# Kernel tuning notes

Measured on AMD Instinct MI355X. Metric: run time of the kernel, lower is better.

## Reference

```python
import jax, jax.numpy as jnp
import numpy as np
from jax import lax

ROUTINGS = 3
SCALING = 2
NUM_CAPSULE = 8
NUM_ATOMS = 16
EPS = 1e-9


def squash(v):
    # SegCaps squash: v * |v|^2 / ((1+|v|^2) * |v|), norm over last axis
    sq = jnp.sum(v * v, axis=-1, keepdims=True)
    return v * sq / ((1.0 + sq) * jnp.sqrt(sq + EPS))


def setup_inputs() -> dict:
    key = jax.random.key(0)
    k1, k2 = jax.random.split(key)
    B, H, Wd, Cin, Ain = 4, 56, 56, 8, 32
    x = jax.random.normal(k1, (B, H, Wd, Cin, Ain), dtype=jnp.float32)
    # TF conv2d_transpose filter layout: [k, k, out_ch, in_ch]
    W = jax.random.normal(k2, (4, 4, NUM_CAPSULE * NUM_ATOMS, Ain), dtype=jnp.float32) * 0.05
    b = 0.1 * jnp.ones((1, 1, NUM_CAPSULE, NUM_ATOMS), dtype=jnp.float32)
    return {"x": x, "W": W, "b": b}


def reference(x, W, b):
    B, H, Wd, Cin, Ain = x.shape
    Cout, Aout = NUM_CAPSULE, NUM_ATOMS
    # [B,H,W,Cin,A] -> [Cin,B,H,W,A] -> [Cin*B,H,W,A]  (faithful to original ordering)
    xt = jnp.transpose(x, (3, 0, 1, 2, 4)).reshape(Cin * B, H, Wd, Ain)
    # TF conv2d_transpose, SAME padding, stride=scaling: out spatial = in * scaling
    out = lax.conv_transpose(
        xt, W, strides=(SCALING, SCALING), padding="SAME",
        dimension_numbers=("NHWC", "HWIO", "NHWC"), transpose_kernel=True)
    Hp, Wp = out.shape[1], out.shape[2]
    # votes: [B, Cin, Hp, Wp, Cout, Aout]  (faithful to original reshape)
    votes = out.reshape(B, Cin, Hp, Wp, Cout, Aout)
    biases = jnp.broadcast_to(b, (Hp, Wp, Cout, Aout))
    logits = jnp.zeros((B, Cin, Hp, Wp, Cout), dtype=x.dtype)
    act = None
    for i in range(ROUTINGS):
        route = jax.nn.softmax(logits, axis=-1)                      # [B,Cin,Hp,Wp,Cout]
        pre = jnp.einsum("bihwc,bihwca->bhwca", route, votes) + biases
        act = squash(pre)                                            # [B,Hp,Wp,Cout,Aout]
        if i < ROUTINGS - 1:
            logits = logits + jnp.einsum("bihwca,bhwca->bihwc", votes, act)
    return act
```

## Files before the change

### kernel.cpp

```cpp
#include <hip/hip_runtime.h>
#include <math.h>

#define CEPS 1e-9f

typedef _Float16 half8 __attribute__((ext_vector_type(8)));
typedef _Float16 h2 __attribute__((ext_vector_type(2)));
typedef __fp16 fp16x2 __attribute__((ext_vector_type(2)));
typedef float floatx16 __attribute__((ext_vector_type(16)));


template<int CTRL>
__device__ __forceinline__ float dpp_add(float v) {
    return v + __int_as_float(__builtin_amdgcn_update_dpp(
        0, __float_as_int(v), CTRL, 0xF, 0xF, false));
}
template<int CTRL>
__device__ __forceinline__ h2 dpp_add_h2(h2 v) {
    int t = __builtin_amdgcn_update_dpp(
        0, __builtin_bit_cast(int, v), CTRL, 0xF, 0xF, false);
    return v + __builtin_bit_cast(h2, t);
}
__device__ __forceinline__ h2 sum_i8_h2(h2 v) {
    v = dpp_add_h2<0xB1>(v);
    v = dpp_add_h2<0x4E>(v);
    v = dpp_add_h2<0x141>(v);
    return v;
}
__device__ __forceinline__ h2 pkrtz(float a, float b) {
    return __builtin_bit_cast(h2, __builtin_amdgcn_cvt_pkrtz(a, b));
}
__device__ __forceinline__ float fdot2(h2 a, h2 b, float c) {
    return __builtin_amdgcn_fdot2(__builtin_bit_cast(fp16x2, a),
                                  __builtin_bit_cast(fp16x2, b), c, false);
}
__device__ __forceinline__ h2 hsel(bool c, h2 a, h2 b) {
    int r = c ? __builtin_bit_cast(int, a) : __builtin_bit_cast(int, b);
    return __builtin_bit_cast(h2, r);
}

__global__ __launch_bounds__(256) void prep_w(const float* __restrict__ Wt,
                                              _Float16* __restrict__ wb) {
    int idx = blockIdx.x * 256 + threadIdx.x;
    int parity = idx >> 11;
    int s = (idx >> 8) & 7;
    int t = (idx >> 6) & 3;
    int l = idx & 63;
    int rh = parity >> 1, rw = parity & 1;
    int n = t * 32 + (l & 31);
    int h = l >> 5;
    int ci0 = ((s & 1) << 4) + (h << 3);
    int kh = ((s >> 2) << 1) + 1 - rh;
    int kw = (((s >> 1) & 1) << 1) + 1 - rw;
    const float* src = Wt + (((kh * 4 + kw) * 128 + n) << 5) + ci0;
    float4 w0 = *(const float4*)src;
    float4 w1 = *(const float4*)(src + 4);
    half8 hv;
    hv[0] = (_Float16)w0.x; hv[1] = (_Float16)w0.y;
    hv[2] = (_Float16)w0.z; hv[3] = (_Float16)w0.w;
    hv[4] = (_Float16)w1.x; hv[5] = (_Float16)w1.y;
    hv[6] = (_Float16)w1.z; hv[7] = (_Float16)w1.w;
    *(half8*)(wb + ((long)idx << 3)) = hv;
}

__global__ __launch_bounds__(256, 5) void caps_mfma(
    const float* __restrict__ x,
    const _Float16* __restrict__ wb,
    const float* __restrict__ bias,
    float* __restrict__ out)
{
    __shared__ __align__(16) unsigned char smem[16000];
    _Float16* xt = (_Float16*)smem;
    _Float16* scxh = (_Float16*)smem;

    const int tid = threadIdx.x;
    const int tile = blockIdx.x;
    const int tu = tile / 14, tv = tile - tu * 14;
    const int u0 = tu * 4, v0 = tv * 4;
    const int rh = blockIdx.y >> 1;
    const int rw = blockIdx.y & 1;
    const int bp = blockIdx.z;
    const _Float16* wsrc = wb + ((long)blockIdx.y << 14);

    #pragma unroll
    for (int it = 0; it < 4; ++it) {
        int idx = tid + (it << 8);
        if (idx < 800) {
            int cell = idx >> 5;
            int r = idx & 31;
            int i = r >> 2;
            int ci0 = (r & 3) << 3;
            int ri = cell / 5, rj = cell - ri * 5;
            int gi = u0 + rh - 1 + ri;
            int gj = v0 + rw - 1 + rj;
            float tmp[8] = {0.f, 0.f, 0.f, 0.f, 0.f, 0.f, 0.f, 0.f};
            if ((unsigned)gi < 56u && (unsigned)gj < 56u) {
                const float* src = x + (((i & 3) * 56 + gi) * 56 + gj) * 256
                                     + ((bp * 2 + (i >> 2)) << 5) + ci0;
                float4 a0 = *(const float4*)src;
                float4 a1 = *(const float4*)(src + 4);
                tmp[0] = a0.x; tmp[1] = a0.y; tmp[2] = a0.z; tmp[3] = a0.w;
                tmp[4] = a1.x; tmp[5] = a1.y; tmp[6] = a1.z; tmp[7] = a1.w;
            }
            half8 hv;
            #pragma unroll
            for (int j = 0; j < 8; ++j) hv[j] = (_Float16)tmp[j];
            *(half8*)(xt + (cell * 8 + i) * 40 + ci0) = hv;
        }
    }
    __syncthreads();

    const int l = tid & 63;
    const int w = tid >> 6;
    const int col = l & 31, h = l >> 5;
    const int invA = (l & 31) * 40 + (h << 3);

    h2 pf[4][8];
    #pragma unroll
    for (int half = 0; half < 2; ++half) {
        floatx16 acc0, acc1;
        #pragma unroll
        for (int j = 0; j < 16; ++j) { acc0[j] = 0.f; acc1[j] = 0.f; }
        const int tb = half << 1;
        #pragma unroll
        for (int s = 0; s < 8; ++s) {
            const int tkh = s >> 2;
            const int tkw = (s >> 1) & 1;
            const int row = w + 1 - tkh;
            int aoff = (row * 5 + 1 - tkw) * 320 + ((s & 1) << 4) + invA;
            asm("" : "+v"(aoff));
            half8 af = *(const half8*)(xt + aoff);
            half8 bf0 = *(const half8*)(wsrc + (((s * 4 + tb) * 64 + l) << 3));
            half8 bf1 = *(const half8*)(wsrc + (((s * 4 + tb + 1) * 64 + l) << 3));
            acc0 = __builtin_amdgcn_mfma_f32_32x32x16_f16(af, bf0, acc0, 0, 0, 0);
            acc1 = __builtin_amdgcn_mfma_f32_32x32x16_f16(af, bf1, acc1, 0, 0, 0);
        }
        #pragma unroll
        for (int m = 0; m < 8; ++m) {
            pf[tb][m]     = pkrtz(acc0[2 * m], acc0[2 * m + 1]);
            pf[tb + 1][m] = pkrtz(acc1[2 * m], acc1[2 * m + 1]);
        }
        __builtin_amdgcn_sched_barrier(0);
    }

    __syncthreads();

    _Float16* scb = scxh + w * (8 * 136);
    const int cI = l >> 3;
    const int iI = l & 7;

    h2 bq2[8];
    {
        const float* bpt = bias + (cI << 4);
        float4 b0 = *(const float4*)bpt;
        float4 b1 = *(const float4*)(bpt + 4);
        float4 b2 = *(const float4*)(bpt + 8);
        float4 b3 = *(const float4*)(bpt + 12);
        bq2[0] = pkrtz(b0.x, b0.y); bq2[1] = pkrtz(b0.z, b0.w);
        bq2[2] = pkrtz(b1.x, b1.y); bq2[3] = pkrtz(b1.z, b1.w);
        bq2[4] = pkrtz(b2.x, b2.y); bq2[5] = pkrtz(b2.z, b2.w);
        bq2[6] = pkrtz(b3.x, b3.y); bq2[7] = pkrtz(b3.z, b3.w);
    }
    const h2 c0125 = pkrtz(0.125f, 0.125f);

    #pragma unroll
    for (int pixl = 0; pixl < 4; ++pixl) {
        #pragma unroll
        for (int t = 0; t < 4; ++t)
            #pragma unroll
            for (int il = 0; il < 4; ++il) {
                h2 pp = pf[t][(pixl << 1) + (il >> 1)];
                _Float16 v = (il & 1) ? pp.y : pp.x;
                scb[((h << 2) + il) * 136 + t * 32 + col] = v;
            }

        const _Float16* rbh = scb + iI * 136 + (cI << 4);
        h2 va2[8];
        *(half8*)&va2[0] = *(const half8*)(rbh);
        *(half8*)&va2[4] = *(const half8*)(rbh + 8);

        h2 pre2[8];
        float lg;

        #pragma unroll
        for (int j = 0; j < 8; ++j) {
            h2 s2 = sum_i8_h2(va2[j]);
            pre2[j] = s2 * c0125 + bq2[j];
        }
        {
            float n0 = fdot2(pre2[0], pre2[0], 0.f);
            float n1 = fdot2(pre2[1], pre2[1], 0.f);
            float n2 = fdot2(pre2[2], pre2[2], 0.f);
            float n3 = fdot2(pre2[3], pre2[3], 0.f);
            n0 = fdot2(pre2[4], pre2[4], n0);
            n1 = fdot2(pre2[5], pre2[5], n1);
            n2 = fdot2(pre2[6], pre2[6], n2);
            n3 = fdot2(pre2[7], pre2[7], n3);
            float nq = (n0 + n1) + (n2 + n3);
            float sc = nq * __builtin_amdgcn_rcpf(1.f + nq)
                          * __builtin_amdgcn_rsqf(nq + CEPS);
            h2 sc2 = pkrtz(sc, sc);
            #pragma unroll
            for (int j = 0; j < 8; ++j) pre2[j] *= sc2;
            float d0 = fdot2(va2[0], pre2[0], 0.f);
            float d1 = fdot2(va2[1], pre2[1], 0.f);
            float d2 = fdot2(va2[2], pre2[2], 0.f);
            float d3 = fdot2(va2[3], pre2[3], 0.f);
            d0 = fdot2(va2[4], pre2[4], d0);
            d1 = fdot2(va2[5], pre2[5], d1);
            d2 = fdot2(va2[6], pre2[6], d2);
            d3 = fdot2(va2[7], pre2[7], d3);
            lg = (d0 + d1) + (d2 + d3);
        }

        #pragma unroll
        for (int r = 1; r < 3; ++r) {
            float e = __expf(lg);
            float ss = dpp_add<0x128>(e);
            ss += __int_as_float(__builtin_amdgcn_ds_swizzle(
                      __float_as_int(ss), 0x401F));
            ss += __shfl_xor(ss, 32);
            float route = e * __builtin_amdgcn_rcpf(ss);
            h2 rt2 = pkrtz(route, route);
            #pragma unroll
            for (int j = 0; j < 8; ++j) {
                h2 p = sum_i8_h2(rt2 * va2[j]);
                pre2[j] = p + bq2[j];
            }
            float n0 = fdot2(pre2[0], pre2[0], 0.f);
            float n1 = fdot2(pre2[1], pre2[1], 0.f);
            float n2 = fdot2(pre2[2], pre2[2], 0.f);
            float n3 = fdot2(pre2[3], pre2[3], 0.f);
            n0 = fdot2(pre2[4], pre2[4], n0);
            n1 = fdot2(pre2[5], pre2[5], n1);
            n2 = fdot2(pre2[6], pre2[6], n2);
            n3 = fdot2(pre2[7], pre2[7], n3);
            float nq = (n0 + n1) + (n2 + n3);
            float sc = nq * __builtin_amdgcn_rcpf(1.f + nq)
                          * __builtin_amdgcn_rsqf(nq + CEPS);
            h2 sc2 = pkrtz(sc, sc);
            #pragma unroll
            for (int j = 0; j < 8; ++j) pre2[j] *= sc2;
            if (r < 2) {
                float d0 = fdot2(va2[0], pre2[0], lg);
                float d1 = fdot2(va2[1], pre2[1], 0.f);
                float d2 = fdot2(va2[2], pre2[2], 0.f);
                float d3 = fdot2(va2[3], pre2[3], 0.f);
                d0 = fdot2(va2[4], pre2[4], d0);
                d1 = fdot2(va2[5], pre2[5], d1);
                d2 = fdot2(va2[6], pre2[6], d2);
                d3 = fdot2(va2[7], pre2[7], d3);
                lg = (d0 + d1) + (d2 + d3);
            }
        }

        if (iI < 4) {
            h2 h0 = hsel((iI & 2) != 0, pre2[4], pre2[0]);
            h2 h1 = hsel((iI & 2) != 0, pre2[5], pre2[1]);
            h2 h2_ = hsel((iI & 2) != 0, pre2[6], pre2[2]);
            h2 h3 = hsel((iI & 2) != 0, pre2[7], pre2[3]);
            h2 p0 = hsel((iI & 1) != 0, h2_, h0);
            h2 p1 = hsel((iI & 1) != 0, h3, h1);
            float4 o4 = make_float4((float)p0.x, (float)p0.y,
                                    (float)p1.x, (float)p1.y);
            const int p = ((u0 + w) << 1) + rh;
            const int q = ((v0 + pixl) << 1) + rw;
            *(float4*)(out + (((bp * 112 + p) * 112 + q) << 7) + cI * 16 + iI * 4) = o4;
        }
    }
}

extern "C" void kernel_launch(void* const* d_in, const int* in_sizes, int n_in,
                              void* d_out, int out_size, void* d_ws, size_t ws_size,
                              hipStream_t stream) {
    const float* x  = (const float*)d_in[0];
    const float* Wt = (const float*)d_in[1];
    const float* b  = (const float*)d_in[2];
    float* out = (float*)d_out;
    _Float16* wb = (_Float16*)d_ws;

    prep_w<<<32, 256, 0, stream>>>(Wt, wb);
    dim3 grid(196, 4, 4);
    caps_mfma<<<grid, 256, 0, stream>>>(x, wb, b, out);
}
```

Before: 120.1 us.

## Remap routing stage so each lane owns half a capsule across all inputs

The routing phase previously handled one pixel at a time per wave, with lanes spread over (capsule, input) and reductions across inputs done by DPP shuffles. Each lane now holds all 8 input votes for half of one output capsule's atoms, covering all four pixels in one pass. Sums over inputs become plain in-register packed adds, and only small DPP steps remain for the atom-half and capsule softmax reductions. This removes the serialized per-pixel loop and many cross-lane ops, at the cost of doubling shared memory to 32 KB, which may lower occupancy, and holding more registers per lane.

```diff
diff --git a/kernel.cpp b/kernel.cpp
--- a/kernel.cpp
+++ b/kernel.cpp
@@ -14,28 +14,12 @@
     return v + __int_as_float(__builtin_amdgcn_update_dpp(
         0, __float_as_int(v), CTRL, 0xF, 0xF, false));
 }
-template<int CTRL>
-__device__ __forceinline__ h2 dpp_add_h2(h2 v) {
-    int t = __builtin_amdgcn_update_dpp(
-        0, __builtin_bit_cast(int, v), CTRL, 0xF, 0xF, false);
-    return v + __builtin_bit_cast(h2, t);
-}
-__device__ __forceinline__ h2 sum_i8_h2(h2 v) {
-    v = dpp_add_h2<0xB1>(v);
-    v = dpp_add_h2<0x4E>(v);
-    v = dpp_add_h2<0x141>(v);
-    return v;
-}
 __device__ __forceinline__ h2 pkrtz(float a, float b) {
     return __builtin_bit_cast(h2, __builtin_amdgcn_cvt_pkrtz(a, b));
 }
 __device__ __forceinline__ float fdot2(h2 a, h2 b, float c) {
     return __builtin_amdgcn_fdot2(__builtin_bit_cast(fp16x2, a),
                                   __builtin_bit_cast(fp16x2, b), c, false);
-}
-__device__ __forceinline__ h2 hsel(bool c, h2 a, h2 b) {
-    int r = c ? __builtin_bit_cast(int, a) : __builtin_bit_cast(int, b);
-    return __builtin_bit_cast(h2, r);
 }
 
 __global__ __launch_bounds__(256) void prep_w(const float* __restrict__ Wt,
@@ -68,7 +52,7 @@
     const float* __restrict__ bias,
     float* __restrict__ out)
 {
-    __shared__ __align__(16) unsigned char smem[16000];
+    __shared__ __align__(16) unsigned char smem[32768];
     _Float16* xt = (_Float16*)smem;
     _Float16* scxh = (_Float16*)smem;
 
@@ -144,128 +128,137 @@
 
     __syncthreads();
 
-    _Float16* scb = scxh + w * (8 * 136);
-    const int cI = l >> 3;
-    const int iI = l & 7;
-
-    h2 bq2[8];
-    {
-        const float* bpt = bias + (cI << 4);
+    _Float16* wbW = scxh + (w << 12);
+    {
+        _Float16* wp = wbW + (h << 9) + col;
+        #pragma unroll
+        for (int t = 0; t < 4; ++t)
+            #pragma unroll
+            for (int m = 0; m < 8; ++m) {
+                h2 pp = pf[t][m];
+                const int pixl = m >> 1;
+                const int il0 = (2 * m) & 3;
+                const int il1 = (2 * m + 1) & 3;
+                wp[pixl * 1024 + il0 * 128 + t * 32] = pp[0];
+                wp[pixl * 1024 + il1 * 128 + t * 32] = pp[1];
+            }
+    }
+
+    const int e = l & 1;
+    const int c = (l >> 1) & 7;
+    const int pl = l >> 4;
+
+    h2 va[8][4];
+    {
+        const _Float16* rp = wbW + (pl << 10) + (c << 4) + (e << 3);
+        #pragma unroll
+        for (int i = 0; i < 8; ++i) {
+            half8 vv = *(const half8*)(rp + (i << 7));
+            va[i][0][0] = vv[0]; va[i][0][1] = vv[1];
+            va[i][1][0] = vv[2]; va[i][1][1] = vv[3];
+            va[i][2][0] = vv[4]; va[i][2][1] = vv[5];
+            va[i][3][0] = vv[6]; va[i][3][1] = vv[7];
+        }
+    }
+
+    h2 bq[4];
+    {
+        const float* bpt = bias + (c << 4) + (e << 3);
         float4 b0 = *(const float4*)bpt;
         float4 b1 = *(const float4*)(bpt + 4);
-        float4 b2 = *(const float4*)(bpt + 8);
-        float4 b3 = *(const float4*)(bpt + 12);
-        bq2[0] = pkrtz(b0.x, b0.y); bq2[1] = pkrtz(b0.z, b0.w);
-        bq2[2] = pkrtz(b1.x, b1.y); bq2[3] = pkrtz(b1.z, b1.w);
-        bq2[4] = pkrtz(b2.x, b2.y); bq2[5] = pkrtz(b2.z, b2.w);
-        bq2[6] = pkrtz(b3.x, b3.y); bq2[7] = pkrtz(b3.z, b3.w);
+        bq[0] = pkrtz(b0.x, b0.y); bq[1] = pkrtz(b0.z, b0.w);
+        bq[2] = pkrtz(b1.x, b1.y); bq[3] = pkrtz(b1.z, b1.w);
     }
     const h2 c0125 = pkrtz(0.125f, 0.125f);
 
-    #pragma unroll
-    for (int pixl = 0; pixl < 4; ++pixl) {
-        #pragma unroll
-        for (int t = 0; t < 4; ++t)
-            #pragma unroll
-            for (int il = 0; il < 4; ++il) {
-                h2 pp = pf[t][(pixl << 1) + (il >> 1)];
-                _Float16 v = (il & 1) ? pp.y : pp.x;
-                scb[((h << 2) + il) * 136 + t * 32 + col] = v;
-            }
-
-        const _Float16* rbh = scb + iI * 136 + (cI << 4);
-        h2 va2[8];
-        *(half8*)&va2[0] = *(const half8*)(rbh);
-        *(half8*)&va2[4] = *(const half8*)(rbh + 8);
-
-        h2 pre2[8];
-        float lg;
-
-        #pragma unroll
-        for (int j = 0; j < 8; ++j) {
-            h2 s2 = sum_i8_h2(va2[j]);
-            pre2[j] = s2 * c0125 + bq2[j];
+    h2 pre[4];
+    float lgv[8];
+
+    #pragma unroll
+    for (int d = 0; d < 4; ++d) {
+        h2 s01 = va[0][d] + va[1][d];
+        h2 s23 = va[2][d] + va[3][d];
+        h2 s45 = va[4][d] + va[5][d];
+        h2 s67 = va[6][d] + va[7][d];
+        h2 s = (s01 + s23) + (s45 + s67);
+        pre[d] = s * c0125 + bq[d];
+    }
+    {
+        float n = fdot2(pre[0], pre[0], 0.f);
+        n = fdot2(pre[1], pre[1], n);
+        n = fdot2(pre[2], pre[2], n);
+        n = fdot2(pre[3], pre[3], n);
+        float nq = dpp_add<0xB1>(n);
+        float sc = nq * __builtin_amdgcn_rcpf(1.f + nq)
+                      * __builtin_amdgcn_rsqf(nq + CEPS);
+        h2 sc2 = pkrtz(sc, sc);
+        #pragma unroll
+        for (int d = 0; d < 4; ++d) pre[d] *= sc2;
+    }
+    #pragma unroll
+    for (int i = 0; i < 8; ++i) {
+        float p = fdot2(va[i][0], pre[0], 0.f);
+        p = fdot2(va[i][1], pre[1], p);
+        p = fdot2(va[i][2], pre[2], p);
+        p = fdot2(va[i][3], pre[3], p);
+        lgv[i] = dpp_add<0xB1>(p);
+    }
+
+    #pragma unroll
+    for (int r = 1; r < 3; ++r) {
+        h2 rt2[8];
+        #pragma unroll
+        for (int i = 0; i < 8; ++i) {
+            float ee = __expf(lgv[i]);
+            float ss = dpp_add<0x4E>(ee);
+            ss = dpp_add<0x141>(ss);
+            ss = dpp_add<0x128>(ss);
+            float route = ee * __builtin_amdgcn_rcpf(ss);
+            rt2[i] = pkrtz(route, route);
+        }
+        #pragma unroll
+        for (int d = 0; d < 4; ++d) {
+            h2 p0 = rt2[0] * va[0][d], p1 = rt2[1] * va[1][d];
+            h2 p2 = rt2[2] * va[2][d], p3 = rt2[3] * va[3][d];
+            h2 p4 = rt2[4] * va[4][d], p5 = rt2[5] * va[5][d];
+            h2 p6 = rt2[6] * va[6][d], p7 = rt2[7] * va[7][d];
+            h2 s = ((p0 + p1) + (p2 + p3)) + ((p4 + p5) + (p6 + p7));
+            pre[d] = s + bq[d];
         }
         {
-            float n0 = fdot2(pre2[0], pre2[0], 0.f);
-            float n1 = fdot2(pre2[1], pre2[1], 0.f);
-            float n2 = fdot2(pre2[2], pre2[2], 0.f);
-            float n3 = fdot2(pre2[3], pre2[3], 0.f);
-            n0 = fdot2(pre2[4], pre2[4], n0);
-            n1 = fdot2(pre2[5], pre2[5], n1);
-            n2 = fdot2(pre2[6], pre2[6], n2);
-            n3 = fdot2(pre2[7], pre2[7], n3);
-            float nq = (n0 + n1) + (n2 + n3);
+            float n = fdot2(pre[0], pre[0], 0.f);
+            n = fdot2(pre[1], pre[1], n);
+            n = fdot2(pre[2], pre[2], n);
+            n = fdot2(pre[3], pre[3], n);
+            float nq = dpp_add<0xB1>(n);
             float sc = nq * __builtin_amdgcn_rcpf(1.f + nq)
                           * __builtin_amdgcn_rsqf(nq + CEPS);
             h2 sc2 = pkrtz(sc, sc);
             #pragma unroll
-            for (int j = 0; j < 8; ++j) pre2[j] *= sc2;
-            float d0 = fdot2(va2[0], pre2[0], 0.f);
-            float d1 = fdot2(va2[1], pre2[1], 0.f);
-            float d2 = fdot2(va2[2], pre2[2], 0.f);
-            float d3 = fdot2(va2[3], pre2[3], 0.f);
-            d0 = fdot2(va2[4], pre2[4], d0);
-            d1 = fdot2(va2[5], pre2[5], d1);
-            d2 = fdot2(va2[6], pre2[6], d2);
-            d3 = fdot2(va2[7], pre2[7], d3);
-            lg = (d0 + d1) + (d2 + d3);
-        }
-
-        #pragma unroll
-        for (int r = 1; r < 3; ++r) {
-            float e = __expf(lg);
-            float ss = dpp_add<0x128>(e);
-            ss += __int_as_float(__builtin_amdgcn_ds_swizzle(
-                      __float_as_int(ss), 0x401F));
-            ss += __shfl_xor(ss, 32);
-            float route = e * __builtin_amdgcn_rcpf(ss);
-            h2 rt2 = pkrtz(route, route);
-            #pragma unroll
-            for (int j = 0; j < 8; ++j) {
-                h2 p = sum_i8_h2(rt2 * va2[j]);
-                pre2[j] = p + bq2[j];
+            for (int d = 0; d < 4; ++d) pre[d] *= sc2;
+        }
+        if (r < 2) {
+            #pragma unroll
+            for (int i = 0; i < 8; ++i) {
+                float p = fdot2(va[i][0], pre[0], 0.f);
+                p = fdot2(va[i][1], pre[1], p);
+                p = fdot2(va[i][2], pre[2], p);
+                p = fdot2(va[i][3], pre[3], p);
+                lgv[i] += dpp_add<0xB1>(p);
             }
-            float n0 = fdot2(pre2[0], pre2[0], 0.f);
-            float n1 = fdot2(pre2[1], pre2[1], 0.f);
-            float n2 = fdot2(pre2[2], pre2[2], 0.f);
-            float n3 = fdot2(pre2[3], pre2[3], 0.f);
-            n0 = fdot2(pre2[4], pre2[4], n0);
-            n1 = fdot2(pre2[5], pre2[5], n1);
-            n2 = fdot2(pre2[6], pre2[6], n2);
-            n3 = fdot2(pre2[7], pre2[7], n3);
-            float nq = (n0 + n1) + (n2 + n3);
-            float sc = nq * __builtin_amdgcn_rcpf(1.f + nq)
-                          * __builtin_amdgcn_rsqf(nq + CEPS);
-            h2 sc2 = pkrtz(sc, sc);
-            #pragma unroll
-            for (int j = 0; j < 8; ++j) pre2[j] *= sc2;
-            if (r < 2) {
-                float d0 = fdot2(va2[0], pre2[0], lg);
-                float d1 = fdot2(va2[1], pre2[1], 0.f);
-                float d2 = fdot2(va2[2], pre2[2], 0.f);
-                float d3 = fdot2(va2[3], pre2[3], 0.f);
-                d0 = fdot2(va2[4], pre2[4], d0);
-                d1 = fdot2(va2[5], pre2[5], d1);
-                d2 = fdot2(va2[6], pre2[6], d2);
-                d3 = fdot2(va2[7], pre2[7], d3);
-                lg = (d0 + d1) + (d2 + d3);
-            }
-        }
-
-        if (iI < 4) {
-            h2 h0 = hsel((iI & 2) != 0, pre2[4], pre2[0]);
-            h2 h1 = hsel((iI & 2) != 0, pre2[5], pre2[1]);
-            h2 h2_ = hsel((iI & 2) != 0, pre2[6], pre2[2]);
-            h2 h3 = hsel((iI & 2) != 0, pre2[7], pre2[3]);
-            h2 p0 = hsel((iI & 1) != 0, h2_, h0);
-            h2 p1 = hsel((iI & 1) != 0, h3, h1);
-            float4 o4 = make_float4((float)p0.x, (float)p0.y,
-                                    (float)p1.x, (float)p1.y);
-            const int p = ((u0 + w) << 1) + rh;
-            const int q = ((v0 + pixl) << 1) + rw;
-            *(float4*)(out + (((bp * 112 + p) * 112 + q) << 7) + cI * 16 + iI * 4) = o4;
-        }
+        }
+    }
+
+    {
+        const int p = ((u0 + w) << 1) + rh;
+        const int q = ((v0 + pl) << 1) + rw;
+        float* op = out + (((bp * 112 + p) * 112 + q) << 7) + (c << 4) + (e << 3);
+        float4 o0 = make_float4((float)pre[0][0], (float)pre[0][1],
+                                (float)pre[1][0], (float)pre[1][1]);
+        float4 o1 = make_float4((float)pre[2][0], (float)pre[2][1],
+                                (float)pre[3][0], (float)pre[3][1]);
+        *(float4*)op = o0;
+        *(float4*)(op + 4) = o1;
     }
 }
 
```

After: 103.3 us (median of 2 runs). 14.0% less time.
